# Performance work log

Hardware: AMD Instinct MI355X
Metric: run time of the kernel (lower is better)

Reference implementation:

```python
import jax, jax.numpy as jnp
import numpy as np

N_TOKEN = 267735
CUTOFF_ENDS = [0, 20000, 40000, 200000, N_TOKEN]
DIV_VAL = 4
D_MODEL = 1024
N_HEAD = 16
D_HEAD = 64
D_INNER = 4096
N_LAYER = 4
QLEN = 512
MLEN = 512
BSZ = 4
EPS = 1e-5


def setup_inputs() -> dict:
    key = jax.random.key(0)
    ks = iter(jax.random.split(key, 40))
    std = 0.02
    inp = {}
    inp["input_ids"] = jax.random.randint(next(ks), (BSZ, QLEN), 0, N_TOKEN)
    inp["mems"] = jax.random.normal(next(ks), (N_LAYER, MLEN, BSZ, D_MODEL), jnp.float32) * std
    # adaptive embedding tables + projections (div_val=4 buckets)
    for i in range(4):
        n = CUTOFF_ENDS[i + 1] - CUTOFF_ENDS[i]
        d = D_MODEL // DIV_VAL ** i
        inp[f"emb{i}"] = jax.random.normal(next(ks), (n, d), jnp.float32) * std
        inp[f"proj{i}"] = jax.random.normal(next(ks), (d, D_MODEL), jnp.float32) * std
    L = N_LAYER
    inp["qkv_w"] = jax.random.normal(next(ks), (L, D_MODEL, 3 * N_HEAD * D_HEAD), jnp.float32) * std
    inp["r_net_w"] = jax.random.normal(next(ks), (L, D_MODEL, N_HEAD * D_HEAD), jnp.float32) * std
    inp["o_w"] = jax.random.normal(next(ks), (L, N_HEAD * D_HEAD, D_MODEL), jnp.float32) * std
    inp["r_w_bias"] = jax.random.normal(next(ks), (L, N_HEAD, D_HEAD), jnp.float32) * std
    inp["r_r_bias"] = jax.random.normal(next(ks), (L, N_HEAD, D_HEAD), jnp.float32) * std
    inp["ln1_g"] = jnp.ones((L, D_MODEL), jnp.float32)
    inp["ln1_b"] = jnp.zeros((L, D_MODEL), jnp.float32)
    inp["ff_w1"] = jax.random.normal(next(ks), (L, D_MODEL, D_INNER), jnp.float32) * std
    inp["ff_b1"] = jnp.zeros((L, D_INNER), jnp.float32)
    inp["ff_w2"] = jax.random.normal(next(ks), (L, D_INNER, D_MODEL), jnp.float32) * std
    inp["ff_b2"] = jnp.zeros((L, D_MODEL), jnp.float32)
    inp["ln2_g"] = jnp.ones((L, D_MODEL), jnp.float32)
    inp["ln2_b"] = jnp.zeros((L, D_MODEL), jnp.float32)
    return inp


def _layer_norm(x, g, b):
    m = x.mean(-1, keepdims=True)
    v = ((x - m) ** 2).mean(-1, keepdims=True)
    return (x - m) * jax.lax.rsqrt(v + EPS) * g + b


def _rel_shift(x):
    # x: (qlen, klen, bsz, n_head)
    q, k, b, n = x.shape
    x = jnp.pad(x, ((0, 0), (1, 0), (0, 0), (0, 0)))
    x = x.reshape(k + 1, q, b, n)[1:]
    return x.reshape(q, k, b, n)


def _adaptive_embed(flat_ids, tables_projs):
    emb = jnp.zeros((flat_ids.shape[0], D_MODEL), jnp.float32)
    for i, (tab, proj) in enumerate(tables_projs):
        l, r = CUTOFF_ENDS[i], CUTOFF_ENDS[i + 1]
        mask = (flat_ids >= l) & (flat_ids < r)
        idx = jnp.clip(flat_ids - l, 0, r - l - 1)
        emb = emb + jnp.where(mask[:, None], tab[idx] @ proj, 0.0)
    return emb * (D_MODEL ** 0.5)


def _forward(input_ids, mems, tables_projs, qkv_w, r_net_w, o_w, r_w_bias, r_r_bias,
             ln1_g, ln1_b, ff_w1, ff_b1, ff_w2, ff_b2, ln2_g, ln2_b):
    ids = input_ids.T  # (qlen, bsz)
    word_emb = _adaptive_embed(ids.reshape(-1), tables_projs).reshape(QLEN, BSZ, D_MODEL)

    klen = MLEN + QLEN
    # masked positions == 1: future tokens only (strictly upper triangular over the q part)
    dec_attn_mask = jnp.concatenate(
        [jnp.zeros((QLEN, MLEN), jnp.float32), jnp.triu(jnp.ones((QLEN, QLEN), jnp.float32), 1)], axis=1
    )[:, :, None, None]  # (qlen, klen, 1, 1)

    pos_seq = jnp.arange(klen - 1, -1, -1, dtype=jnp.float32)
    inv_freq = 1.0 / (10000.0 ** (jnp.arange(0, D_MODEL, 2, dtype=jnp.float32) / D_MODEL))
    sin_inp = pos_seq[:, None] * inv_freq[None, :]
    pos_emb = jnp.concatenate([jnp.sin(sin_inp), jnp.cos(sin_inp)], axis=-1)  # (klen, d_model)

    scale = 1.0 / (D_HEAD ** 0.5)
    h = word_emb
    for l in range(N_LAYER):
        cat = jnp.concatenate([mems[l], h], axis=0)              # (klen, bsz, d)
        w_heads = cat @ qkv_w[l]                                  # (klen, bsz, 3*nh*dh)
        wq, wk, wv = jnp.split(w_heads, 3, axis=-1)
        q = wq[-QLEN:].reshape(QLEN, BSZ, N_HEAD, D_HEAD)
        k = wk.reshape(klen, BSZ, N_HEAD, D_HEAD)
        v = wv.reshape(klen, BSZ, N_HEAD, D_HEAD)
        rk = (pos_emb @ r_net_w[l]).reshape(klen, N_HEAD, D_HEAD)
        AC = jnp.einsum('ibnd,jbnd->ijbn', q + r_w_bias[l], k)
        BD = _rel_shift(jnp.einsum('ibnd,jnd->ijbn', q + r_r_bias[l], rk))
        score = (AC + BD) * scale
        score = score * (1.0 - dec_attn_mask) - 1e30 * dec_attn_mask
        prob = jax.nn.softmax(score, axis=1)
        attn_vec = jnp.einsum('ijbn,jbnd->ibnd', prob, v).reshape(QLEN, BSZ, N_HEAD * D_HEAD)
        h = _layer_norm(h + attn_vec @ o_w[l], ln1_g[l], ln1_b[l])
        core = jax.nn.relu(h @ ff_w1[l] + ff_b1[l]) @ ff_w2[l] + ff_b2[l]
        h = _layer_norm(h + core, ln2_g[l], ln2_b[l])
    return jnp.transpose(h, (1, 0, 2))  # (bsz, qlen, d_model)


def reference(input_ids, mems, emb0, proj0, emb1, proj1, emb2, proj2, emb3, proj3,
              qkv_w, r_net_w, o_w, r_w_bias, r_r_bias, ln1_g, ln1_b,
              ff_w1, ff_b1, ff_w2, ff_b2, ln2_g, ln2_b):
    tables_projs = [(emb0, proj0), (emb1, proj1), (emb2, proj2), (emb3, proj3)]
    return _forward(input_ids, mems, tables_projs, qkv_w, r_net_w, o_w, r_w_bias, r_r_bias,
                    ln1_g, ln1_b, ff_w1, ff_b1, ff_w2, ff_b2, ln2_g, ln2_b)
```

## Files before the change

### kernel.cpp

```cpp
#include <hip/hip_runtime.h>
#include <hip/hip_bf16.h>

typedef __attribute__((ext_vector_type(8))) short short8;
typedef __attribute__((ext_vector_type(4))) float f32x4;
typedef __hip_bfloat16 bf16;

#define QLEN 512
#define MLEN 512
#define KLEN 1024
#define BSZ  4
#define DM   1024
#define NH   16
#define DH   64
#define DI   4096
#define NL   4
#define KEMB 1408

__device__ __forceinline__ void gload16(const bf16* g, const void* l) {
  __builtin_amdgcn_global_load_lds(
      (const __attribute__((address_space(1))) void*)g,
      (__attribute__((address_space(3))) void*)l, 16, 0, 0);
}

__device__ __forceinline__ bf16 bits2bf(short s) { bf16 h; *(short*)&h = s; return h; }

__global__ __launch_bounds__(256) void embA_kernel(
    const int* __restrict__ ids,
    const float* __restrict__ e0, const float* __restrict__ e1,
    const float* __restrict__ e2, const float* __restrict__ e3,
    bf16* __restrict__ Aemb)
{
  const int t = blockIdx.x;
  const int q = t >> 2, b = t & 3;
  const int id = ids[b * QLEN + q];
  const float* tab; int d, off, koff;
  if (id < 20000)       { tab = e0; d = 1024; off = 0;      koff = 0; }
  else if (id < 40000)  { tab = e1; d = 256;  off = 20000;  koff = 1024; }
  else if (id < 200000) { tab = e2; d = 64;   off = 40000;  koff = 1280; }
  else                  { tab = e3; d = 16;   off = 200000; koff = 1344; }
  bf16* row = Aemb + (long)t * KEMB;
  const float* tr = tab + (long)(id - off) * d;
  for (int k = threadIdx.x; k < KEMB; k += 256) {
    const int kk = k - koff;
    float v = 0.f;
    if (kk >= 0 && kk < d) v = tr[kk];
    row[k] = __float2bfloat16(v);
  }
}

__global__ __launch_bounds__(256) void projT_kernel(
    const float* __restrict__ p0, const float* __restrict__ p1,
    const float* __restrict__ p2, const float* __restrict__ p3,
    bf16* __restrict__ out)
{
  __shared__ float t[32][33];
  const int k0 = blockIdx.x * 32, n0 = blockIdx.y * 32;
  const int nx = threadIdx.x & 31, ky = threadIdx.x >> 5;
#pragma unroll
  for (int p = 0; p < 4; ++p) {
    const int k = k0 + ky + p * 8;
    float v = 0.f;
    if (k < 1024)       v = p0[(long)k * 1024 + n0 + nx];
    else if (k < 1280)  v = p1[(long)(k - 1024) * 1024 + n0 + nx];
    else if (k < 1344)  v = p2[(long)(k - 1280) * 1024 + n0 + nx];
    else if (k < 1360)  v = p3[(long)(k - 1344) * 1024 + n0 + nx];
    t[ky + p * 8][nx] = v;
  }
  __syncthreads();
#pragma unroll
  for (int p = 0; p < 4; ++p)
    out[(long)(n0 + ky + p * 8) * KEMB + k0 + nx] = __float2bfloat16(t[nx][ky + p * 8]);
}

__global__ __launch_bounds__(256) void embsum_kernel(const float* __restrict__ part,
                                                     float* __restrict__ h, bf16* __restrict__ cat)
{
  const long i = ((long)blockIdx.x * 256 + threadIdx.x) * 4;
  const float4 a = *(const float4*)(part + i);
  const float4 b = *(const float4*)(part + 2097152 + i);
  float4 s; s.x = a.x + b.x; s.y = a.y + b.y; s.z = a.z + b.z; s.w = a.w + b.w;
  *(float4*)(h + i) = s;
  bf16* cr = cat + (long)2048 * 1024 + i;
  cr[0] = __float2bfloat16(s.x); cr[1] = __float2bfloat16(s.y);
  cr[2] = __float2bfloat16(s.z); cr[3] = __float2bfloat16(s.w);
}

__global__ __launch_bounds__(256) void posemb_kernel(bf16* __restrict__ pe)
{
  const int j = blockIdx.x;
  const float pos = (float)(KLEN - 1 - j);
  for (int i = threadIdx.x; i < DM / 2; i += 256) {
    const float freq = expf(-9.210340371976184f * ((float)(2 * i) / (float)DM));
    const float ang = pos * freq;
    pe[(long)j * DM + i]          = __float2bfloat16(sinf(ang));
    pe[(long)j * DM + DM / 2 + i] = __float2bfloat16(cosf(ang));
  }
}

__global__ __launch_bounds__(256) void wtrans_kernel(const float* __restrict__ in,
                                                     bf16* __restrict__ out, int R, int C)
{
  __shared__ float t[32][33];
  in  += (long)blockIdx.z * R * C;
  out += (long)blockIdx.z * R * C;
  const int c0 = blockIdx.x * 32, r0 = blockIdx.y * 32;
  const int cx = threadIdx.x & 31, ry = threadIdx.x >> 5;
#pragma unroll
  for (int p = 0; p < 4; ++p)
    t[ry + p * 8][cx] = in[(long)(r0 + ry + p * 8) * C + c0 + cx];
  __syncthreads();
#pragma unroll
  for (int p = 0; p < 4; ++p)
    out[(long)(c0 + ry + p * 8) * R + r0 + cx] = __float2bfloat16(t[cx][ry + p * 8]);
}

__global__ __launch_bounds__(256) void memsconv_kernel(const float* __restrict__ mems,
                                                       bf16* __restrict__ cat0)
{
  const long i = ((long)blockIdx.x * 256 + threadIdx.x) * 4;
  const long l = i >> 21, rem = i & ((1 << 21) - 1);
  const float4 v = *(const float4*)(mems + i);
  bf16* dst = cat0 + l * 4194304 + rem;
  dst[0] = __float2bfloat16(v.x); dst[1] = __float2bfloat16(v.y);
  dst[2] = __float2bfloat16(v.z); dst[3] = __float2bfloat16(v.w);
}

template<int BM, int BN>
__global__ __launch_bounds__(256) void gemm_bf16(
    const bf16* __restrict__ A, long aStrB, long aStrN, int lda,
    const bf16* __restrict__ B, long bStrB, long bStrN, int ldb,
    void* __restrict__ C, long cStrB, long cStrN, int ldc,
    int K, float scale, const float* __restrict__ bias, long biasStrB, long biasStrN,
    int flags, int zN, int zSplit, long cSplitStr)
{
  constexpr int RA = BM / 64, RB = BN / 64, FM = BM / 32, FN = BN / 32;
  __shared__ __align__(16) bf16 As[2][BM * 32];
  __shared__ __align__(16) bf16 Bs[2][BN * 32];
  const int zc = blockIdx.z % zSplit, zt = blockIdx.z / zSplit;
  const int zn = zt % zN, zb = zt / zN;
  A += (long)zb * aStrB + (long)zn * aStrN + (long)zc * K;
  B += (long)zb * bStrB + (long)zn * bStrN + (long)zc * K;
  const int tid = threadIdx.x, lane = tid & 63;
  const int w = tid >> 6, wr = w >> 1, wc = w & 1;
  const int m0 = blockIdx.y * BM, n0 = blockIdx.x * BN;
  const int l15 = lane & 15, l4 = lane >> 4;
  const int rowS = tid >> 2;
  const int cbS  = (tid & 3) * 16;
  const int swS  = cbS ^ (((rowS >> 1) & 3) << 4);
  const int wbase = w * 1024;
  const bf16* Ast = A + (size_t)(m0 + rowS) * lda + (swS >> 1);
  const bf16* Bst = B + (size_t)(n0 + rowS) * ldb + (swS >> 1);

#define STAGE_TILE(buf, kk)                                                       \
  {                                                                               \
    _Pragma("unroll")                                                             \
    for (int r = 0; r < RA; ++r)                                                  \
      gload16(Ast + (size_t)(r * 64) * lda + (kk), (char*)As[buf] + r * 4096 + wbase); \
    _Pragma("unroll")                                                             \
    for (int r = 0; r < RB; ++r)                                                  \
      gload16(Bst + (size_t)(r * 64) * ldb + (kk), (char*)Bs[buf] + r * 4096 + wbase); \
  }

  f32x4 acc[FM][FN] = {};
  STAGE_TILE(0, 0)
  asm volatile("s_waitcnt vmcnt(0)" ::: "memory");
  __syncthreads();
  int cur = 0;
  for (int k0 = 0; k0 < K; k0 += 32) {
    if (k0 + 32 < K) {
      if (cur == 0) STAGE_TILE(1, k0 + 32)
      else          STAGE_TILE(0, k0 + 32)
    }
    short8 af[FM], bfr[FN];
#pragma unroll
    for (int f = 0; f < FM; ++f) {
      const int row = wr * (BM / 2) + f * 16 + l15;
      af[f] = *(const short8*)((char*)As[cur] + row * 64 + ((16 * l4) ^ (((row >> 1) & 3) << 4)));
    }
#pragma unroll
    for (int f = 0; f < FN; ++f) {
      const int row = wc * (BN / 2) + f * 16 + l15;
      bfr[f] = *(const short8*)((char*)Bs[cur] + row * 64 + ((16 * l4) ^ (((row >> 1) & 3) << 4)));
    }
#pragma unroll
    for (int fm = 0; fm < FM; ++fm)
#pragma unroll
      for (int fn = 0; fn < FN; ++fn)
        acc[fm][fn] = __builtin_amdgcn_mfma_f32_16x16x32_bf16(af[fm], bfr[fn], acc[fm][fn], 0, 0, 0);
    asm volatile("s_waitcnt vmcnt(0)" ::: "memory");
    __syncthreads();
    cur ^= 1;
  }
#undef STAGE_TILE
  const int outbf = flags & 1, relu = flags & 4;
#pragma unroll
  for (int fm = 0; fm < FM; ++fm) {
#pragma unroll
    for (int fn = 0; fn < FN; ++fn) {
      const int col = n0 + wc * (BN / 2) + fn * 16 + l15;
      const int rw0 = m0 + wr * (BM / 2) + fm * 16 + l4 * 4;
      const float bv = (bias && zc == 0) ? bias[(size_t)zb * biasStrB + (size_t)zn * biasStrN + col] : 0.f;
#pragma unroll
      for (int r = 0; r < 4; ++r) {
        float v = (acc[fm][fn][r] + bv) * scale;
        if (relu) v = fmaxf(v, 0.f);
        const int row = rw0 + r;
        const size_t cOff = (size_t)zb * cStrB + (size_t)zn * cStrN + (size_t)zc * cSplitStr;
        if (outbf) {
          ((bf16*)C + cOff)[(size_t)row * ldc + col] = __float2bfloat16(v);
        } else {
          ((float*)C + cOff)[(size_t)row * ldc + col] = v;
        }
      }
    }
  }
}

__global__ __launch_bounds__(256) void vt_kernel(const bf16* __restrict__ wh, bf16* __restrict__ vt)
{
  const int bn = blockIdx.y, b = bn >> 4, n = bn & 15;
  const int j0 = blockIdx.x * 64;
  __shared__ bf16 t[64][72];
  const bf16* src = wh + (size_t)b * 3072 + 2048 + n * 64;
  const int tid = threadIdx.x;
#pragma unroll
  for (int r = 0; r < 16; ++r) {
    const int jl = r * 4 + (tid >> 6), d = tid & 63;
    t[jl][d] = src[(size_t)(j0 + jl) * 12288 + d];
  }
  __syncthreads();
  bf16* dst = vt + (size_t)bn * 64 * KLEN;
#pragma unroll
  for (int r = 0; r < 16; ++r) {
    const int d = r * 4 + (tid >> 6), j = tid & 63;
    dst[(size_t)d * KLEN + j0 + j] = t[j][d];
  }
}

__global__ __launch_bounds__(256) void fattn_kernel(
    const bf16* __restrict__ wh,
    const bf16* __restrict__ rkb_l,
    const bf16* __restrict__ vt,
    const float* __restrict__ rwb,
    const float* __restrict__ rrb,
    float* __restrict__ po, float* __restrict__ pm, float* __restrict__ pl)
{
  const int q0 = blockIdx.x * 64;
  const int bn = blockIdx.y, b = bn >> 4, n = bn & 15;
  const int ck = blockIdx.z;
  const int tid = threadIdx.x, w = tid >> 6, lane = tid & 63;
  const int l15 = lane & 15, l4 = lane >> 4;
  __shared__ float Tl[4][16][84];
  __shared__ bf16  Pl[4][16][72];

  short8 qa[2], qb[2];
  {
    const bf16* qp = wh + (size_t)(2048 + b) * 3072 + (size_t)(q0 + 16 * w + l15) * 12288 + n * 64;
#pragma unroll
    for (int kk = 0; kk < 2; ++kk) {
      const short8 qv = *(const short8*)(qp + kk * 32 + 8 * l4);
      const float* wv = rwb + n * 64 + kk * 32 + 8 * l4;
      const float* rv = rrb + n * 64 + kk * 32 + 8 * l4;
      short8 a, c;
#pragma unroll
      for (int e = 0; e < 8; ++e) {
        const float q = __bfloat162float(bits2bf(qv[e]));
        const bf16 ab = __float2bfloat16(q + wv[e]);
        const bf16 cb = __float2bfloat16(q + rv[e]);
        a[e] = *(const short*)&ab;  c[e] = *(const short*)&cb;
      }
      qa[kk] = a; qb[kk] = c;
    }
  }

  const bf16* kbase = wh + (size_t)b * 3072 + 1024 + n * 64;
  const bf16* vbase = vt + (size_t)bn * 65536;
  const int ntiles = 9 + (q0 >> 6);
  const int pb0 = -q0 + 496 - 16 * w;

  f32x4 accO[4] = {};
  float mrow[4] = { -1e30f, -1e30f, -1e30f, -1e30f };
  float lrow[4] = { 0.f, 0.f, 0.f, 0.f };

  for (int t = ck; t < ntiles; t += 2) {
    const int j0 = t * 64;
    f32x4 S[4] = {};
#pragma unroll
    for (int fn = 0; fn < 4; ++fn)
#pragma unroll
      for (int kk = 0; kk < 2; ++kk) {
        const short8 kf = *(const short8*)(kbase + (size_t)(j0 + 16 * fn + l15) * 12288 + kk * 32 + 8 * l4);
        S[fn] = __builtin_amdgcn_mfma_f32_16x16x32_bf16(qa[kk], kf, S[fn], 0, 0, 0);
      }
    {
      f32x4 T[5] = {};
#pragma unroll
      for (int ftl = 0; ftl < 5; ++ftl) {
        const int p = pb0 + j0 + 16 * ftl + l15;
#pragma unroll
        for (int kk = 0; kk < 2; ++kk) {
          const short8 rf = *(const short8*)(rkb_l + (size_t)p * 1024 + n * 64 + kk * 32 + 8 * l4);
          T[ftl] = __builtin_amdgcn_mfma_f32_16x16x32_bf16(qb[kk], rf, T[ftl], 0, 0, 0);
        }
      }
#pragma unroll
      for (int ftl = 0; ftl < 5; ++ftl)
#pragma unroll
        for (int r = 0; r < 4; ++r)
          Tl[w][4 * l4 + r][16 * ftl + l15] = T[ftl][r];
    }
    const bool fullvalid = (j0 + 63) <= (512 + q0);
    float sv[4][4];
#pragma unroll
    for (int fn = 0; fn < 4; ++fn)
#pragma unroll
      for (int r = 0; r < 4; ++r) {
        const int il = 4 * l4 + r;
        const float tshift = Tl[w][il][16 * fn + l15 + 15 - il];
        const float s = (S[fn][r] + tshift) * 0.125f;
        const bool valid = fullvalid || (j0 + 16 * fn + l15 - 512 <= q0 + 16 * w + il);
        sv[fn][r] = valid ? s : -1e30f;
      }
    float pv[4][4];
#pragma unroll
    for (int r = 0; r < 4; ++r) {
      float m4 = fmaxf(fmaxf(sv[0][r], sv[1][r]), fmaxf(sv[2][r], sv[3][r]));
      m4 = fmaxf(m4, __shfl_xor(m4, 1));
      m4 = fmaxf(m4, __shfl_xor(m4, 2));
      m4 = fmaxf(m4, __shfl_xor(m4, 4));
      m4 = fmaxf(m4, __shfl_xor(m4, 8));
      const float mn = fmaxf(mrow[r], m4);
      const float alpha = expf(mrow[r] - mn);
      mrow[r] = mn;
      float ps = 0.f;
#pragma unroll
      for (int fn = 0; fn < 4; ++fn) {
        const float e = expf(sv[fn][r] - mn);
        pv[fn][r] = e; ps += e;
      }
      ps += __shfl_xor(ps, 1);
      ps += __shfl_xor(ps, 2);
      ps += __shfl_xor(ps, 4);
      ps += __shfl_xor(ps, 8);
      lrow[r] = lrow[r] * alpha + ps;
#pragma unroll
      for (int fd = 0; fd < 4; ++fd) accO[fd][r] *= alpha;
    }
#pragma unroll
    for (int fn = 0; fn < 4; ++fn)
#pragma unroll
      for (int r = 0; r < 4; ++r)
        Pl[w][4 * l4 + r][16 * fn + l15] = __float2bfloat16(pv[fn][r]);
    short8 pa[2];
    pa[0] = *(const short8*)&Pl[w][l15][8 * l4];
    pa[1] = *(const short8*)&Pl[w][l15][32 + 8 * l4];
#pragma unroll
    for (int fd = 0; fd < 4; ++fd)
#pragma unroll
      for (int kk = 0; kk < 2; ++kk) {
        const short8 vf = *(const short8*)(vbase + (size_t)(16 * fd + l15) * 1024 + j0 + kk * 32 + 8 * l4);
        accO[fd] = __builtin_amdgcn_mfma_f32_16x16x32_bf16(pa[kk], vf, accO[fd], 0, 0, 0);
      }
  }
  const int cb = ck * 64 + bn;
  float* pob = po + (size_t)cb * 512 * 64;
#pragma unroll
  for (int fd = 0; fd < 4; ++fd)
#pragma unroll
    for (int r = 0; r < 4; ++r) {
      const int row = q0 + 16 * w + 4 * l4 + r;
      pob[(size_t)row * 64 + 16 * fd + l15] = accO[fd][r];
    }
  if (l15 == 0) {
#pragma unroll
    for (int r = 0; r < 4; ++r) {
      const int row = q0 + 16 * w + 4 * l4 + r;
      pm[(size_t)cb * 512 + row] = mrow[r];
      pl[(size_t)cb * 512 + row] = lrow[r];
    }
  }
}

__global__ __launch_bounds__(256) void fmerge_kernel(
    const float* __restrict__ po, const float* __restrict__ pm,
    const float* __restrict__ pl, bf16* __restrict__ av)
{
  const long i = ((long)blockIdx.x * 256 + threadIdx.x) * 4;
  const long bnq = i >> 6;
  const int d4 = (int)(i & 63);
  const int bn = (int)(bnq >> 9), q = (int)(bnq & 511);
  const int b = bn >> 4, n = bn & 15;
  const float m0 = pm[bnq], m1 = pm[32768 + bnq];
  const float l0 = pl[bnq], l1 = pl[32768 + bnq];
  const float m = fmaxf(m0, m1);
  const float w0 = expf(m0 - m), w1 = expf(m1 - m);
  const float inv = 1.f / (w0 * l0 + w1 * l1);
  const float4 o0 = *(const float4*)(po + bnq * 64 + d4);
  const float4 o1 = *(const float4*)(po + 2097152 + bnq * 64 + d4);
  bf16* dst = av + (size_t)(q * 4 + b) * 1024 + n * 64 + d4;
  dst[0] = __float2bfloat16((w0 * o0.x + w1 * o1.x) * inv);
  dst[1] = __float2bfloat16((w0 * o0.y + w1 * o1.y) * inv);
  dst[2] = __float2bfloat16((w0 * o0.z + w1 * o1.z) * inv);
  dst[3] = __float2bfloat16((w0 * o0.w + w1 * o1.w) * inv);
}

__global__ __launch_bounds__(256) void add_ln_kernel(
    float* __restrict__ h,
    const float* __restrict__ x0, const float* __restrict__ x1,
    const float* __restrict__ g, const float* __restrict__ bb, bf16* __restrict__ cat)
{
  float* hr = h + (long)blockIdx.x * DM;
  const long o = (long)blockIdx.x * DM;
  bf16* cr = cat + (long)(2048 + blockIdx.x) * DM;
  const int tid = threadIdx.x;
  __shared__ float red[256];
  float v0 = hr[tid]       + x0[o + tid]       + x1[o + tid];
  float v1 = hr[tid + 256] + x0[o + tid + 256] + x1[o + tid + 256];
  float v2 = hr[tid + 512] + x0[o + tid + 512] + x1[o + tid + 512];
  float v3 = hr[tid + 768] + x0[o + tid + 768] + x1[o + tid + 768];
  red[tid] = v0 + v1 + v2 + v3; __syncthreads();
  for (int off = 128; off; off >>= 1) { if (tid < off) red[tid] += red[tid + off]; __syncthreads(); }
  const float mean = red[0] * (1.f / DM); __syncthreads();
  const float d0 = v0 - mean, d1 = v1 - mean, d2 = v2 - mean, d3 = v3 - mean;
  red[tid] = d0 * d0 + d1 * d1 + d2 * d2 + d3 * d3; __syncthreads();
  for (int off = 128; off; off >>= 1) { if (tid < off) red[tid] += red[tid + off]; __syncthreads(); }
  const float inv = rsqrtf(red[0] * (1.f / DM) + 1e-5f);
  const float o0 = d0 * inv * g[tid]       + bb[tid];
  const float o1 = d1 * inv * g[tid + 256] + bb[tid + 256];
  const float o2 = d2 * inv * g[tid + 512] + bb[tid + 512];
  const float o3 = d3 * inv * g[tid + 768] + bb[tid + 768];
  hr[tid]       = o0;  cr[tid]       = __float2bfloat16(o0);
  hr[tid + 256] = o1;  cr[tid + 256] = __float2bfloat16(o1);
  hr[tid + 512] = o2;  cr[tid + 512] = __float2bfloat16(o2);
  hr[tid + 768] = o3;  cr[tid + 768] = __float2bfloat16(o3);
}

__global__ __launch_bounds__(256) void out_kernel(const float* __restrict__ h, float* __restrict__ out)
{
  const int t = blockIdx.x, q = t >> 2, b = t & 3;
  const float* hr = h + (long)t * DM;
  float* orow = out + ((long)b * QLEN + q) * DM;
  for (int s = 0; s < 4; ++s) orow[threadIdx.x + 256 * s] = hr[threadIdx.x + 256 * s];
}

extern "C" void kernel_launch(void* const* d_in, const int* in_sizes, int n_in,
                              void* d_out, int out_size, void* d_ws, size_t ws_size,
                              hipStream_t stream)
{
  const int*   ids  = (const int*)d_in[0];
  const float* mems = (const float*)d_in[1];
  const float* e0 = (const float*)d_in[2]; const float* p0 = (const float*)d_in[3];
  const float* e1 = (const float*)d_in[4]; const float* p1 = (const float*)d_in[5];
  const float* e2 = (const float*)d_in[6]; const float* p2 = (const float*)d_in[7];
  const float* e3 = (const float*)d_in[8]; const float* p3 = (const float*)d_in[9];
  const float* qkvw = (const float*)d_in[10];
  const float* rnet = (const float*)d_in[11];
  const float* ow   = (const float*)d_in[12];
  const float* rwb  = (const float*)d_in[13];
  const float* rrb  = (const float*)d_in[14];
  const float* ln1g = (const float*)d_in[15];
  const float* ln1b = (const float*)d_in[16];
  const float* fw1  = (const float*)d_in[17];
  const float* fb1  = (const float*)d_in[18];
  const float* fw2  = (const float*)d_in[19];
  const float* fb2  = (const float*)d_in[20];
  const float* ln2g = (const float*)d_in[21];
  const float* ln2b = (const float*)d_in[22];
  float* out = (float*)d_out;

  char* p = (char*)d_ws;
  float* h    = (float*)p;            p += (size_t)2048 * 1024 * 4;
  bf16*  cat0 = (bf16*)p;             p += (size_t)5 * 4096 * 1024 * 2;
  bf16*  pe   = (bf16*)p;             p += (size_t)1024 * 1024 * 2;
  bf16*  rkb  = (bf16*)p;             p += (size_t)4 * 1024 * 1024 * 2;
  bf16*  wh   = (bf16*)p;             p += (size_t)4096 * 3072 * 2;
  bf16*  vt   = (bf16*)p;             p += (size_t)64 * 64 * 1024 * 2;
  bf16*  qkvT = (bf16*)p;             p += (size_t)4 * 3072 * 1024 * 2;
  bf16*  rnT  = (bf16*)p;             p += (size_t)4 * 1024 * 1024 * 2;
  bf16*  oT   = (bf16*)p;             p += (size_t)4 * 1024 * 1024 * 2;
  bf16*  f1T  = (bf16*)p;             p += (size_t)4 * 4096 * 1024 * 2;
  bf16*  f2T  = (bf16*)p;             p += (size_t)4 * 4096 * 1024 * 2;
  bf16*  mid  = (bf16*)p;
  float* partE= (float*)p;
  p += (size_t)4 * 16 * 512 * 1024 * 2;
  bf16*  Aemb = (bf16*)p;
  bf16*  projT= (bf16*)(p + (size_t)2048 * KEMB * 2);
  float* partP= (float*)p;
  float* po   = (float*)p;
  float* pm   = (float*)(p + (size_t)16 * 1024 * 1024);
  float* pl   = (float*)(p + (size_t)17 * 1024 * 1024);
  p += (size_t)4 * 16 * 512 * 1024 * 2;
  bf16*  av   = (bf16*)p;             p += (size_t)2048 * 1024 * 2;

  embA_kernel<<<2048, 256, 0, stream>>>(ids, e0, e1, e2, e3, Aemb);
  projT_kernel<<<dim3(KEMB / 32, 32), 256, 0, stream>>>(p0, p1, p2, p3, projT);
  gemm_bf16<128, 64><<<dim3(16, 16, 2), 256, 0, stream>>>(
      Aemb, 0, 0, KEMB, projT, 0, 0, KEMB, partE, 0, 0, 1024,
      KEMB / 2, 32.f, nullptr, 0, 0, 0, 1, 2, 2097152);
  embsum_kernel<<<2048, 256, 0, stream>>>(partE, h, cat0);
  posemb_kernel<<<1024, 256, 0, stream>>>(pe);
  memsconv_kernel<<<8192, 256, 0, stream>>>(mems, cat0);

  wtrans_kernel<<<dim3(96, 32, 4), 256, 0, stream>>>(qkvw, qkvT, DM, 3072);
  wtrans_kernel<<<dim3(32, 32, 4), 256, 0, stream>>>(rnet, rnT, DM, DM);
  wtrans_kernel<<<dim3(32, 32, 4), 256, 0, stream>>>(ow, oT, DM, DM);
  wtrans_kernel<<<dim3(128, 32, 4), 256, 0, stream>>>(fw1, f1T, DM, DI);
  wtrans_kernel<<<dim3(32, 128, 4), 256, 0, stream>>>(fw2, f2T, DI, DM);

  gemm_bf16<128, 128><<<dim3(8, 8, 4), 256, 0, stream>>>(
      pe, 0, 0, 1024, rnT, 1048576, 0, 1024, rkb, 1048576, 0, 1024,
      1024, 1.f, nullptr, 0, 0, 1, 1, 1, 0);

  for (int l = 0; l < NL; ++l) {
    bf16* catl = cat0 + (size_t)l * 4194304;
    gemm_bf16<128, 128><<<dim3(24, 32, 1), 256, 0, stream>>>(
        catl, 0, 0, 1024, qkvT + (size_t)l * 3145728, 0, 0, 1024, wh, 0, 0, 3072,
        1024, 1.f, nullptr, 0, 0, 1, 1, 1, 0);

    vt_kernel<<<dim3(16, 64), 256, 0, stream>>>(wh, vt);

    fattn_kernel<<<dim3(8, 64, 2), 256, 0, stream>>>(
        wh, rkb + (size_t)l * 1048576, vt,
        rwb + l * NH * DH, rrb + l * NH * DH, po, pm, pl);
    fmerge_kernel<<<2048, 256, 0, stream>>>(po, pm, pl, av);

    gemm_bf16<128, 64><<<dim3(16, 16, 2), 256, 0, stream>>>(
        av, 0, 0, 1024, oT + (size_t)l * 1048576, 0, 0, 1024, partP, 0, 0, 1024,
        512, 1.f, nullptr, 0, 0, 0, 1, 2, 2097152);
    add_ln_kernel<<<2048, 256, 0, stream>>>(h, partP, partP + 2097152,
                                            ln1g + l * DM, ln1b + l * DM, catl);

    gemm_bf16<128, 128><<<dim3(32, 16, 1), 256, 0, stream>>>(
        catl + (size_t)2048 * 1024, 0, 0, 1024, f1T + (size_t)l * 4194304, 0, 0, 1024,
        mid, 0, 0, 4096, 1024, 1.f, fb1 + (size_t)l * DI, 0, 0, 1 | 4, 1, 1, 0);
    gemm_bf16<128, 64><<<dim3(16, 16, 2), 256, 0, stream>>>(
        mid, 0, 0, 4096, f2T + (size_t)l * 4194304, 0, 0, 4096, partP, 0, 0, 1024,
        2048, 1.f, fb2 + (size_t)l * DM, 0, 0, 0, 1, 2, 2097152);
    add_ln_kernel<<<2048, 256, 0, stream>>>(h, partP, partP + 2097152,
                                            ln2g + l * DM, ln2b + l * DM,
                                            cat0 + (size_t)(l + 1) * 4194304);
  }

  out_kernel<<<2048, 256, 0, stream>>>(h, out);
}
```

Before: 1.142 ms.

## Pack K contiguously per head, split attention KV into four chunks, reorder grid

```diff
diff --git a/kernel.cpp b/kernel.cpp
--- a/kernel.cpp
+++ b/kernel.cpp
@@ -216,17 +216,21 @@
   }
 }
 
-__global__ __launch_bounds__(256) void vt_kernel(const bf16* __restrict__ wh, bf16* __restrict__ vt)
+__global__ __launch_bounds__(256) void vt_kernel(const bf16* __restrict__ wh,
+                                                 bf16* __restrict__ vt, bf16* __restrict__ kb)
 {
   const int bn = blockIdx.y, b = bn >> 4, n = bn & 15;
   const int j0 = blockIdx.x * 64;
   __shared__ bf16 t[64][72];
   const bf16* src = wh + (size_t)b * 3072 + 2048 + n * 64;
+  const bf16* ksrc = wh + (size_t)b * 3072 + 1024 + n * 64;
+  bf16* kdst = kb + (size_t)bn * 65536;
   const int tid = threadIdx.x;
 #pragma unroll
   for (int r = 0; r < 16; ++r) {
     const int jl = r * 4 + (tid >> 6), d = tid & 63;
     t[jl][d] = src[(size_t)(j0 + jl) * 12288 + d];
+    kdst[(size_t)(j0 + jl) * 64 + d] = ksrc[(size_t)(j0 + jl) * 12288 + d];
   }
   __syncthreads();
   bf16* dst = vt + (size_t)bn * 64 * KLEN;
@@ -239,14 +243,15 @@
 
 __global__ __launch_bounds__(256) void fattn_kernel(
     const bf16* __restrict__ wh,
+    const bf16* __restrict__ kb,
     const bf16* __restrict__ rkb_l,
     const bf16* __restrict__ vt,
     const float* __restrict__ rwb,
     const float* __restrict__ rrb,
     float* __restrict__ po, float* __restrict__ pm, float* __restrict__ pl)
 {
-  const int q0 = blockIdx.x * 64;
-  const int bn = blockIdx.y, b = bn >> 4, n = bn & 15;
+  const int bn = blockIdx.x, b = bn >> 4, n = bn & 15;
+  const int q0 = blockIdx.y * 64;
   const int ck = blockIdx.z;
   const int tid = threadIdx.x, w = tid >> 6, lane = tid & 63;
   const int l15 = lane & 15, l4 = lane >> 4;
@@ -273,7 +278,7 @@
     }
   }
 
-  const bf16* kbase = wh + (size_t)b * 3072 + 1024 + n * 64;
+  const bf16* kbase = kb + (size_t)bn * 65536;
   const bf16* vbase = vt + (size_t)bn * 65536;
   const int ntiles = 9 + (q0 >> 6);
   const int pb0 = -q0 + 496 - 16 * w;
@@ -282,14 +287,14 @@
   float mrow[4] = { -1e30f, -1e30f, -1e30f, -1e30f };
   float lrow[4] = { 0.f, 0.f, 0.f, 0.f };
 
-  for (int t = ck; t < ntiles; t += 2) {
+  for (int t = ck; t < ntiles; t += 4) {
     const int j0 = t * 64;
     f32x4 S[4] = {};
 #pragma unroll
     for (int fn = 0; fn < 4; ++fn)
 #pragma unroll
       for (int kk = 0; kk < 2; ++kk) {
-        const short8 kf = *(const short8*)(kbase + (size_t)(j0 + 16 * fn + l15) * 12288 + kk * 32 + 8 * l4);
+        const short8 kf = *(const short8*)(kbase + (size_t)(j0 + 16 * fn + l15) * 64 + kk * 32 + 8 * l4);
         S[fn] = __builtin_amdgcn_mfma_f32_16x16x32_bf16(qa[kk], kf, S[fn], 0, 0, 0);
       }
     {
@@ -390,18 +395,25 @@
   const int d4 = (int)(i & 63);
   const int bn = (int)(bnq >> 9), q = (int)(bnq & 511);
   const int b = bn >> 4, n = bn & 15;
-  const float m0 = pm[bnq], m1 = pm[32768 + bnq];
-  const float l0 = pl[bnq], l1 = pl[32768 + bnq];
-  const float m = fmaxf(m0, m1);
-  const float w0 = expf(m0 - m), w1 = expf(m1 - m);
-  const float inv = 1.f / (w0 * l0 + w1 * l1);
-  const float4 o0 = *(const float4*)(po + bnq * 64 + d4);
-  const float4 o1 = *(const float4*)(po + 2097152 + bnq * 64 + d4);
+  float mv[4], lv[4];
+#pragma unroll
+  for (int c = 0; c < 4; ++c) { mv[c] = pm[c * 32768 + bnq]; lv[c] = pl[c * 32768 + bnq]; }
+  const float m = fmaxf(fmaxf(mv[0], mv[1]), fmaxf(mv[2], mv[3]));
+  float wv[4], den = 0.f;
+#pragma unroll
+  for (int c = 0; c < 4; ++c) { wv[c] = expf(mv[c] - m); den += wv[c] * lv[c]; }
+  const float inv = 1.f / den;
+  float4 o = { 0.f, 0.f, 0.f, 0.f };
+#pragma unroll
+  for (int c = 0; c < 4; ++c) {
+    const float4 oc = *(const float4*)(po + (size_t)c * 2097152 + bnq * 64 + d4);
+    o.x += wv[c] * oc.x; o.y += wv[c] * oc.y; o.z += wv[c] * oc.z; o.w += wv[c] * oc.w;
+  }
   bf16* dst = av + (size_t)(q * 4 + b) * 1024 + n * 64 + d4;
-  dst[0] = __float2bfloat16((w0 * o0.x + w1 * o1.x) * inv);
-  dst[1] = __float2bfloat16((w0 * o0.y + w1 * o1.y) * inv);
-  dst[2] = __float2bfloat16((w0 * o0.z + w1 * o1.z) * inv);
-  dst[3] = __float2bfloat16((w0 * o0.w + w1 * o1.w) * inv);
+  dst[0] = __float2bfloat16(o.x * inv);
+  dst[1] = __float2bfloat16(o.y * inv);
+  dst[2] = __float2bfloat16(o.z * inv);
+  dst[3] = __float2bfloat16(o.w * inv);
 }
 
 __global__ __launch_bounds__(256) void add_ln_kernel(
@@ -475,6 +487,7 @@
   bf16*  rkb  = (bf16*)p;             p += (size_t)4 * 1024 * 1024 * 2;
   bf16*  wh   = (bf16*)p;             p += (size_t)4096 * 3072 * 2;
   bf16*  vt   = (bf16*)p;             p += (size_t)64 * 64 * 1024 * 2;
+  bf16*  kb   = (bf16*)p;             p += (size_t)64 * 1024 * 64 * 2;
   bf16*  qkvT = (bf16*)p;             p += (size_t)4 * 3072 * 1024 * 2;
   bf16*  rnT  = (bf16*)p;             p += (size_t)4 * 1024 * 1024 * 2;
   bf16*  oT   = (bf16*)p;             p += (size_t)4 * 1024 * 1024 * 2;
@@ -487,8 +500,8 @@
   bf16*  projT= (bf16*)(p + (size_t)2048 * KEMB * 2);
   float* partP= (float*)p;
   float* po   = (float*)p;
-  float* pm   = (float*)(p + (size_t)16 * 1024 * 1024);
-  float* pl   = (float*)(p + (size_t)17 * 1024 * 1024);
+  float* pm   = (float*)(p + (size_t)32 * 1024 * 1024);
+  float* pl   = (float*)(p + (size_t)33 * 1024 * 1024);
   p += (size_t)4 * 16 * 512 * 1024 * 2;
   bf16*  av   = (bf16*)p;             p += (size_t)2048 * 1024 * 2;
 
@@ -517,10 +530,10 @@
         catl, 0, 0, 1024, qkvT + (size_t)l * 3145728, 0, 0, 1024, wh, 0, 0, 3072,
         1024, 1.f, nullptr, 0, 0, 1, 1, 1, 0);
 
-    vt_kernel<<<dim3(16, 64), 256, 0, stream>>>(wh, vt);
-
-    fattn_kernel<<<dim3(8, 64, 2), 256, 0, stream>>>(
-        wh, rkb + (size_t)l * 1048576, vt,
+    vt_kernel<<<dim3(16, 64), 256, 0, stream>>>(wh, vt, kb);
+
+    fattn_kernel<<<dim3(64, 8, 4), 256, 0, stream>>>(
+        wh, kb, rkb + (size_t)l * 1048576, vt,
         rwb + l * NH * DH, rrb + l * NH * DH, po, pm, pl);
     fmerge_kernel<<<2048, 256, 0, stream>>>(po, pm, pl, av);
 
```

Result: no change. 1.159 ms (+1.5%).
